# Kernel optimization log

Measured on AMD Instinct MI355X. Metric: run time of the kernel, lower is better.

Reference implementation:

```python
import jax, jax.numpy as jnp
import numpy as np

DIM = 384; HEADS = 12; WS = 7; SHIFT = 3
IMG_H = 56; IMG_W = 56; B = 32; MLP_HID = 1536
N = WS * WS; HEAD_DIM = DIM // HEADS


def _rel_pos_index():
    # standard Swin relative position index, shape [N, N], values in [0, (2*WS-1)^2)
    coords = np.stack(np.meshgrid(np.arange(WS), np.arange(WS), indexing='ij')).reshape(2, -1)
    rel = (coords[:, :, None] - coords[:, None, :]).transpose(1, 2, 0)
    rel[..., 0] += WS - 1
    rel[..., 1] += WS - 1
    rel[..., 0] *= 2 * WS - 1
    return jnp.asarray(rel.sum(-1))

REL_IDX = _rel_pos_index()


def _shift_mask():
    # Swin shifted-window attention mask: 0 within region, -100 across regions
    img = np.zeros((IMG_H, IMG_W))
    cnt = 0
    for hs in (slice(0, -WS), slice(-WS, -SHIFT), slice(-SHIFT, None)):
        for ws_ in (slice(0, -WS), slice(-WS, -SHIFT), slice(-SHIFT, None)):
            img[hs, ws_] = cnt
            cnt += 1
    mw = img.reshape(IMG_H // WS, WS, IMG_W // WS, WS).transpose(0, 2, 1, 3).reshape(-1, N)
    am = mw[:, None, :] - mw[:, :, None]
    return jnp.asarray(np.where(am != 0, -100.0, 0.0).astype(np.float32))


def setup_inputs() -> dict:
    key = jax.random.key(0)
    ks = jax.random.split(key, 8)
    rn = lambda k, s: jax.random.normal(k, s, jnp.float32) * 0.02
    return {
        'x': jax.random.normal(ks[0], (B, IMG_H * IMG_W, DIM), jnp.float32),
        'mask': _shift_mask(),
        'w_ln1': jnp.ones((DIM,), jnp.float32), 'b_ln1': jnp.zeros((DIM,), jnp.float32),
        'w_qkv': rn(ks[1], (3 * DIM, DIM)), 'b_qkv': jnp.zeros((3 * DIM,), jnp.float32),
        'rel_bias': rn(ks[2], ((2 * WS - 1) ** 2, HEADS)),
        'w_proj': rn(ks[3], (DIM, DIM)), 'b_proj': jnp.zeros((DIM,), jnp.float32),
        'w_ln2': jnp.ones((DIM,), jnp.float32), 'b_ln2': jnp.zeros((DIM,), jnp.float32),
        'w_fc1': rn(ks[4], (MLP_HID, DIM)), 'b_fc1': jnp.zeros((MLP_HID,), jnp.float32),
        'w_fc2': rn(ks[5], (DIM, MLP_HID)), 'b_fc2': jnp.zeros((DIM,), jnp.float32),
        'H': IMG_H, 'W': IMG_W,
    }


def _ln(x, g, b, eps=1e-5):
    mu = x.mean(-1, keepdims=True)
    var = ((x - mu) ** 2).mean(-1, keepdims=True)
    return (x - mu) * jax.lax.rsqrt(var + eps) * g + b


def reference(x, mask, w_ln1, b_ln1, w_qkv, b_qkv, rel_bias, w_proj, b_proj,
              w_ln2, b_ln2, w_fc1, b_fc1, w_fc2, b_fc2, H, W):
    Bsz, L, C = x.shape
    nW = (H // WS) * (W // WS)
    shortcut = x
    h = _ln(x, w_ln1, b_ln1).reshape(Bsz, H, W, C)
    # cyclic shift
    h = jnp.roll(h, (-SHIFT, -SHIFT), axis=(1, 2))
    # window partition -> [B*nW, N, C]
    h = h.reshape(Bsz, H // WS, WS, W // WS, WS, C).transpose(0, 1, 3, 2, 4, 5).reshape(-1, N, C)
    nB = h.shape[0]
    qkv = (h @ w_qkv.T + b_qkv).reshape(nB, N, 3, HEADS, HEAD_DIM).transpose(2, 0, 3, 1, 4)
    q, k, v = qkv[0] * (HEAD_DIM ** -0.5), qkv[1], qkv[2]  # each [nB, heads, N, hd]
    attn = jnp.einsum('bhnd,bhmd->bhnm', q, k)
    bias = rel_bias[REL_IDX].transpose(2, 0, 1)  # [heads, N, N]
    attn = attn + bias[None]
    attn = attn.reshape(Bsz, nW, HEADS, N, N) + mask[None, :, None]
    attn = jax.nn.softmax(attn, axis=-1).reshape(nB, HEADS, N, N)
    o = jnp.einsum('bhnm,bhmd->bhnd', attn, v).transpose(0, 2, 1, 3).reshape(nB, N, C)
    o = o @ w_proj.T + b_proj
    # window reverse
    o = o.reshape(Bsz, H // WS, W // WS, WS, WS, C).transpose(0, 1, 3, 2, 4, 5).reshape(Bsz, H, W, C)
    o = jnp.roll(o, (SHIFT, SHIFT), axis=(1, 2)).reshape(Bsz, H * W, C)
    x = shortcut + o
    h2 = _ln(x, w_ln2, b_ln2)
    h2 = jax.nn.gelu(h2 @ w_fc1.T + b_fc1) @ w_fc2.T + b_fc2
    return x + h2
```

## Files before the change

### kernel.cpp

```cpp
#include <hip/hip_runtime.h>
#include <stdint.h>

#define B_     32
#define IMG    56
#define L_     (IMG*IMG)
#define C_     384
#define HEADS_ 12
#define HD     32
#define WS_    7
#define N_     49
#define NWIN   64
#define NB     (B_*NWIN)
#define M_TOK  (NB*N_)
#define QKVF   1152

typedef __attribute__((ext_vector_type(8))) short bf16x8;
typedef __attribute__((ext_vector_type(4))) float f32x4;
typedef __attribute__((ext_vector_type(4))) unsigned short u16x4;

__device__ __forceinline__ float bf2f(unsigned short u) {
  union { unsigned int u; float f; } c; c.u = ((unsigned int)u) << 16; return c.f;
}
__device__ __forceinline__ unsigned short f2bf(float f) {
  union { float f; unsigned int u; } c; c.f = f;
  unsigned int r = c.u + 0x7FFFu + ((c.u >> 16) & 1u);
  return (unsigned short)(r >> 16);
}

__device__ __forceinline__ void gload_lds16(const void* g, void* l) {
  __builtin_amdgcn_global_load_lds(
      (const __attribute__((address_space(1))) unsigned int*)(uintptr_t)g,
      (__attribute__((address_space(3))) unsigned int*)(uintptr_t)l,
      16, 0, 0);
}

#define MFMA16(a, b, c) __builtin_amdgcn_mfma_f32_16x16x32_bf16((a), (b), (c), 0, 0, 0)

__global__ __launch_bounds__(256) void k_prep(
    const float* __restrict__ w_qkv, const float* __restrict__ w_proj,
    const float* __restrict__ w_fc1, const float* __restrict__ w_fc2,
    const float* __restrict__ relb,  const float* __restrict__ mask,
    ushort* __restrict__ wbq, ushort* __restrict__ wbp,
    ushort* __restrict__ wb1, ushort* __restrict__ wb2,
    ushort* __restrict__ bm)
{
  int g = blockIdx.x * 256 + threadIdx.x;
  if (g < 442368)        { wbq[g]            = f2bf(w_qkv[g]); return; }
  if (g < 589824)        { wbp[g - 442368]   = f2bf(w_proj[g - 442368]); return; }
  if (g < 1179648)       { wb1[g - 589824]   = f2bf(w_fc1[g - 589824]); return; }
  if (g < 1769472)       { wb2[g - 1179648]  = f2bf(w_fc2[g - 1179648]); return; }
  int n = g - 1769472;
  int r    = n & 3;
  int col  = (n >> 2) & 63;
  int quad = (n >> 8) & 3;
  int i    = (n >> 10) & 3;
  int hw   = n >> 12;
  int h = hw % HEADS_, wc = hw / HEADS_;
  int row = i * 16 + quad * 4 + r;
  float v;
  if (col >= N_) v = -30000.f;
  else if (row >= N_) v = 0.f;
  else {
    int idx = (row / WS_ - col / WS_ + 6) * 13 + (row % WS_ - col % WS_ + 6);
    v = relb[idx * HEADS_ + h] + mask[((size_t)wc * N_ + row) * N_ + col];
  }
  bm[n] = f2bf(v);
}

template<bool WINDOW>
__global__ __launch_bounds__(256) void k_ln(const float* __restrict__ X,
    const float* __restrict__ G, const float* __restrict__ Bb,
    ushort* __restrict__ out)
{
  int token = blockIdx.x * 4 + (threadIdx.x >> 6);
  int lane  = threadIdx.x & 63;
  const float* xp = X + (size_t)token * C_;
  float v[6];
#pragma unroll
  for (int t = 0; t < 6; t++) v[t] = xp[lane + 64*t];
  float s = 0.f, s2 = 0.f;
#pragma unroll
  for (int t = 0; t < 6; t++) { s += v[t]; s2 += v[t]*v[t]; }
#pragma unroll
  for (int off = 32; off > 0; off >>= 1) {
    s  += __shfl_down(s,  off, 64);
    s2 += __shfl_down(s2, off, 64);
  }
  s = __shfl(s, 0, 64); s2 = __shfl(s2, 0, 64);
  float mu   = s * (1.f / C_);
  float rstd = rsqrtf(s2 * (1.f / C_) - mu * mu + 1e-5f);
  size_t obase;
  if (WINDOW) {
    int b = token / L_, pix = token % L_;
    int hi = pix / IMG, wj = pix % IMG;
    int sh = hi - 3; if (sh < 0) sh += IMG;
    int sw = wj - 3; if (sw < 0) sw += IMG;
    int w = b * NWIN + (sh / WS_) * 8 + (sw / WS_);
    int p = (sh % WS_) * WS_ + (sw % WS_);
    obase = ((size_t)w * N_ + p) * C_;
  } else {
    obase = (size_t)token * C_;
  }
#pragma unroll
  for (int t = 0; t < 6; t++) {
    int c = lane + 64*t;
    out[obase + c] = f2bf((v[t] - mu) * rstd * G[c] + Bb[c]);
  }
}

template<int EPI, typename OutT>
__global__ __launch_bounds__(256, 2) void k_gemm(
    const ushort* __restrict__ A, const ushort* __restrict__ W,
    const float* __restrict__ bias, OutT* __restrict__ out,
    const float* __restrict__ res, int M, int N, int K)
{
  __shared__ __align__(16) ushort As[3][256*32];
  __shared__ __align__(16) ushort Bs[3][128*32];
  int ntn = N >> 7;
  int nwg = gridDim.x;
  int bid = (blockIdx.x & 7) * (nwg >> 3) + (blockIdx.x >> 3);
  int m0 = (bid / ntn) << 8;
  int n0 = (bid % ntn) << 7;
  int tid  = threadIdx.x;
  int wave = tid >> 6, lane = tid & 63;
  int l15  = lane & 15, quad = lane >> 4;
  int wm = (wave >> 1) << 7;
  int wn = (wave & 1) << 6;

  int srow = tid >> 2;
  int scol = (tid & 3) * 8;
  const ushort* gA = A + (size_t)(m0 + srow) * K + scol;
  const ushort* gB = W + (size_t)(n0 + srow) * K + scol;
  int oA = srow * 32 + scol;

  f32x4 acc[8][4];
#pragma unroll
  for (int i = 0; i < 8; i++)
#pragma unroll
    for (int j = 0; j < 4; j++) acc[i][j] = (f32x4){0.f, 0.f, 0.f, 0.f};

#pragma unroll
  for (int it = 0; it < 4; it++)
    gload_lds16(gA + (size_t)it * 64 * K, &As[0][oA + it * 2048]);
#pragma unroll
  for (int it = 0; it < 2; it++)
    gload_lds16(gB + (size_t)it * 64 * K, &Bs[0][oA + it * 2048]);
  gA += 32; gB += 32;
#pragma unroll
  for (int it = 0; it < 4; it++)
    gload_lds16(gA + (size_t)it * 64 * K, &As[1][oA + it * 2048]);
#pragma unroll
  for (int it = 0; it < 2; it++)
    gload_lds16(gB + (size_t)it * 64 * K, &Bs[1][oA + it * 2048]);
  gA += 32; gB += 32;

  int nt = K >> 5;
  int cur = 0, stg = 2;
  for (int t = 0; t < nt; t++) {
    if (t + 1 < nt) asm volatile("s_waitcnt vmcnt(6)" ::: "memory");
    else            asm volatile("s_waitcnt vmcnt(0)" ::: "memory");
    asm volatile("s_barrier" ::: "memory");
    if (t + 2 < nt) {
#pragma unroll
      for (int it = 0; it < 4; it++)
        gload_lds16(gA + (size_t)it * 64 * K, &As[stg][oA + it * 2048]);
#pragma unroll
      for (int it = 0; it < 2; it++)
        gload_lds16(gB + (size_t)it * 64 * K, &Bs[stg][oA + it * 2048]);
      gA += 32; gB += 32;
    }
    bf16x8 af[8], bfr[4];
#pragma unroll
    for (int i = 0; i < 8; i++) af[i]  = *(const bf16x8*)&As[cur][(wm + i*16 + l15)*32 + quad*8];
#pragma unroll
    for (int j = 0; j < 4; j++) bfr[j] = *(const bf16x8*)&Bs[cur][(wn + j*16 + l15)*32 + quad*8];
    __builtin_amdgcn_s_setprio(1);
#pragma unroll
    for (int i = 0; i < 8; i++)
#pragma unroll
      for (int j = 0; j < 4; j++)
        acc[i][j] = MFMA16(af[i], bfr[j], acc[i][j]);
    __builtin_amdgcn_s_setprio(0);
    cur = (cur == 2) ? 0 : cur + 1;
    stg = (stg == 2) ? 0 : stg + 1;
  }

  float bv[4];
#pragma unroll
  for (int j = 0; j < 4; j++) bv[j] = bias[n0 + wn + j*16 + l15];
#pragma unroll
  for (int i = 0; i < 8; i++) {
#pragma unroll
    for (int r = 0; r < 4; r++) {
      int row = m0 + wm + i*16 + quad*4 + r;
      size_t dstbase;
      if (EPI == 1) {
        int w = row / N_, p = row % N_;
        int b = w >> 6, wi = w & 63;
        int hi = (wi >> 3) * WS_ + p / WS_ + 3; if (hi >= IMG) hi -= IMG;
        int wj = (wi & 7)  * WS_ + p % WS_ + 3; if (wj >= IMG) wj -= IMG;
        dstbase = ((size_t)b * L_ + hi * IMG + wj) * C_;
      } else {
        dstbase = (size_t)row * N;
      }
#pragma unroll
      for (int j = 0; j < 4; j++) {
        int col = n0 + wn + j*16 + l15;
        float v = acc[i][j][r] + bv[j];
        if (EPI == 2) {
          float e = __expf(-1.5957691216057308f * (v + 0.044715f * v * v * v));
          v = v * __builtin_amdgcn_rcpf(1.f + e);
        }
        size_t dst = dstbase + col;
        if (EPI == 1) v += res[dst];
        if (EPI == 3) v += res[(size_t)row * N + col];
        if constexpr (sizeof(OutT) == 4) out[dst] = v;
        else                             out[dst] = f2bf(v);
      }
    }
  }
}

__global__ __launch_bounds__(256, 3) void k_attn_mfma(
    const ushort* __restrict__ qkv, const ushort* __restrict__ bm,
    ushort* __restrict__ out)
{
  __shared__ __align__(16) ushort Ps[4][64*64];
  __shared__ __align__(16) ushort Vt[4][32*64];
  int wave = threadIdx.x >> 6, lane = threadIdx.x & 63;
  int task = blockIdx.x * 4 + wave;
  int w = task / HEADS_, h = task % HEADS_;
  int l15 = lane & 15, quad = lane >> 4;

  const ushort* base = qkv + (size_t)w * N_ * QKVF + h * HD;

  bf16x8 qf[4], kf[4];
#pragma unroll
  for (int i = 0; i < 4; i++) {
    int rr = i * 16 + l15; if (rr > 48) rr = 48;
    const ushort* rp = base + (size_t)rr * QKVF + quad * 8;
    qf[i] = *(const bf16x8*)rp;
    kf[i] = *(const bf16x8*)(rp + C_);
  }

  {
    int m = lane > 48 ? 48 : lane;
    const ushort* vp = base + (size_t)m * QKVF + 2 * C_;
    bf16x8 v0 = *(const bf16x8*)vp;
    bf16x8 v1 = *(const bf16x8*)(vp + 8);
    bf16x8 v2 = *(const bf16x8*)(vp + 16);
    bf16x8 v3 = *(const bf16x8*)(vp + 24);
    ushort* vt = &Vt[wave][0];
#pragma unroll
    for (int d = 0; d < 32; d++) {
      ushort val = (ushort)(d < 8 ? v0[d & 7] : d < 16 ? v1[d & 7]
                                  : d < 24 ? v2[d & 7] : v3[d & 7]);
      vt[d * 64 + (lane ^ ((d & 7) << 3))] = val;
    }
  }

  f32x4 acc[4][4];
#pragma unroll
  for (int i = 0; i < 4; i++)
#pragma unroll
    for (int j = 0; j < 4; j++) acc[i][j] = (f32x4){0.f, 0.f, 0.f, 0.f};
#pragma unroll
  for (int i = 0; i < 4; i++)
#pragma unroll
    for (int j = 0; j < 4; j++)
      acc[i][j] = MFMA16(qf[i], kf[j], acc[i][j]);

  const ushort* bmb = bm + ((size_t)(w & 63) * HEADS_ + h) * 4096;
  float sv[4][4][4];
#pragma unroll
  for (int i = 0; i < 4; i++)
#pragma unroll
    for (int j = 0; j < 4; j++) {
      u16x4 bv = *(const u16x4*)(bmb + (((i * 4 + quad) * 64) + (j * 16 + l15)) * 4);
#pragma unroll
      for (int r = 0; r < 4; r++)
        sv[i][j][r] = acc[i][j][r] * 0.17677669529663687f + bf2f(bv[r]);
    }

  float mx[4][4], sm[4][4];
#pragma unroll
  for (int i = 0; i < 4; i++)
#pragma unroll
    for (int r = 0; r < 4; r++)
      mx[i][r] = fmaxf(fmaxf(sv[i][0][r], sv[i][1][r]),
                       fmaxf(sv[i][2][r], sv[i][3][r]));
#pragma unroll
  for (int off = 1; off <= 8; off <<= 1)
#pragma unroll
    for (int i = 0; i < 4; i++)
#pragma unroll
      for (int r = 0; r < 4; r++)
        mx[i][r] = fmaxf(mx[i][r], __shfl_xor(mx[i][r], off, 64));
#pragma unroll
  for (int i = 0; i < 4; i++)
#pragma unroll
    for (int r = 0; r < 4; r++) sm[i][r] = 0.f;
#pragma unroll
  for (int i = 0; i < 4; i++)
#pragma unroll
    for (int j = 0; j < 4; j++)
#pragma unroll
      for (int r = 0; r < 4; r++) {
        float e = __expf(sv[i][j][r] - mx[i][r]);
        sv[i][j][r] = e;
        sm[i][r] += e;
      }
#pragma unroll
  for (int off = 1; off <= 8; off <<= 1)
#pragma unroll
    for (int i = 0; i < 4; i++)
#pragma unroll
      for (int r = 0; r < 4; r++)
        sm[i][r] += __shfl_xor(sm[i][r], off, 64);

  ushort* pw = &Ps[wave][0];
#pragma unroll
  for (int i = 0; i < 4; i++)
#pragma unroll
    for (int r = 0; r < 4; r++) {
      float inv = __builtin_amdgcn_rcpf(sm[i][r]);
      int row = i * 16 + quad * 4 + r;
      int s = (row & 7) << 3;
#pragma unroll
      for (int j = 0; j < 4; j++)
        pw[row * 64 + ((j * 16 + l15) ^ s)] = f2bf(sv[i][j][r] * inv);
    }

  f32x4 o[4][2];
#pragma unroll
  for (int i = 0; i < 4; i++)
#pragma unroll
    for (int jv = 0; jv < 2; jv++) o[i][jv] = (f32x4){0.f, 0.f, 0.f, 0.f};
  const ushort* vt = &Vt[wave][0];
#pragma unroll
  for (int ks = 0; ks < 2; ks++) {
    int kc = ks * 32 + quad * 8;
    bf16x8 pa[4], vb[2];
#pragma unroll
    for (int i = 0; i < 4; i++) {
      int row = i * 16 + l15;
      pa[i] = *(const bf16x8*)&pw[row * 64 + (kc ^ ((row & 7) << 3))];
    }
#pragma unroll
    for (int jv = 0; jv < 2; jv++) {
      int nn = jv * 16 + l15;
      vb[jv] = *(const bf16x8*)&vt[nn * 64 + (kc ^ ((nn & 7) << 3))];
    }
#pragma unroll
    for (int i = 0; i < 4; i++)
#pragma unroll
      for (int jv = 0; jv < 2; jv++)
        o[i][jv] = MFMA16(pa[i], vb[jv], o[i][jv]);
  }

  ushort* op = out + ((size_t)w * N_) * C_ + h * HD;
#pragma unroll
  for (int i = 0; i < 4; i++)
#pragma unroll
    for (int r = 0; r < 4; r++) {
      int row = i * 16 + quad * 4 + r;
      if (row < N_) {
#pragma unroll
        for (int jv = 0; jv < 2; jv++)
          op[(size_t)row * C_ + jv * 16 + l15] = f2bf(o[i][jv][r]);
      }
    }
}

extern "C" void kernel_launch(void* const* d_in, const int* in_sizes, int n_in,
                              void* d_out, int out_size, void* d_ws, size_t ws_size,
                              hipStream_t stream) {
  (void)in_sizes; (void)n_in; (void)out_size; (void)ws_size;
  const float* x      = (const float*)d_in[0];
  const float* mask   = (const float*)d_in[1];
  const float* w_ln1  = (const float*)d_in[2];
  const float* b_ln1  = (const float*)d_in[3];
  const float* w_qkv  = (const float*)d_in[4];
  const float* b_qkv  = (const float*)d_in[5];
  const float* relb   = (const float*)d_in[6];
  const float* w_proj = (const float*)d_in[7];
  const float* b_proj = (const float*)d_in[8];
  const float* w_ln2  = (const float*)d_in[9];
  const float* b_ln2  = (const float*)d_in[10];
  const float* w_fc1  = (const float*)d_in[11];
  const float* b_fc1  = (const float*)d_in[12];
  const float* w_fc2  = (const float*)d_in[13];
  const float* b_fc2  = (const float*)d_in[14];

  char* ws = (char*)d_ws;
  ushort* r0 = (ushort*)ws;
  ushort* r1 = (ushort*)(ws + 308281344);
  ushort* bmt = (ushort*)(ws + 231211008);
  ushort* wbq = (ushort*)(ws + 385351680);
  ushort* wbp = wbq + QKVF * C_;
  ushort* wb1 = wbp + C_ * C_;
  ushort* wb2 = wb1 + 1536 * C_;
  float*  x1   = (float*)d_out;
  float*  outp = (float*)d_out;

  k_prep<<<4915200/256, 256, 0, stream>>>(w_qkv, w_proj, w_fc1, w_fc2,
                                          relb, mask, wbq, wbp, wb1, wb2, bmt);

  k_ln<true ><<<M_TOK/4, 256, 0, stream>>>(x, w_ln1, b_ln1, r1);
  k_gemm<0, ushort><<<(M_TOK/256)*(QKVF/128), 256, 0, stream>>>(
      r1, wbq, b_qkv, r0, nullptr, M_TOK, QKVF, 384);
  k_attn_mfma<<<NB*HEADS_/4, 256, 0, stream>>>(r0, bmt, r1);
  k_gemm<1, float><<<(M_TOK/256)*(C_/128), 256, 0, stream>>>(
      r1, wbp, b_proj, x1, x, M_TOK, C_, 384);
  k_ln<false><<<M_TOK/4, 256, 0, stream>>>(x1, w_ln2, b_ln2, r1);
  k_gemm<2, ushort><<<(M_TOK/256)*(1536/128), 256, 0, stream>>>(
      r1, wb1, b_fc1, r0, nullptr, M_TOK, 1536, 384);
  k_gemm<3, float><<<(M_TOK/256)*(C_/128), 256, 0, stream>>>(
      r0, wb2, b_fc2, outp, x1, M_TOK, C_, 1536);
}
```

Measured before the change: 1.030 ms.

## Load GEMM A operand directly from global into registers, bypassing LDS

The GEMM kernel no longer stages the A tile through shared memory. Each wave loads its A fragments straight from global memory into double-buffered registers, while B stays on a 3-stage LDS ring. This cuts LDS capacity and LDS read traffic for A and may raise occupancy. In exchange it adds register pressure and uncoalesced 16-byte global loads per lane, with hand-tuned vmcnt waits that must match the number of loads in flight.

```diff
diff --git a/kernel.cpp b/kernel.cpp
--- a/kernel.cpp
+++ b/kernel.cpp
@@ -114,7 +114,6 @@
     const float* __restrict__ bias, OutT* __restrict__ out,
     const float* __restrict__ res, int M, int N, int K)
 {
-  __shared__ __align__(16) ushort As[3][256*32];
   __shared__ __align__(16) ushort Bs[3][128*32];
   int ntn = N >> 7;
   int nwg = gridDim.x;
@@ -129,9 +128,10 @@
 
   int srow = tid >> 2;
   int scol = (tid & 3) * 8;
-  const ushort* gA = A + (size_t)(m0 + srow) * K + scol;
   const ushort* gB = W + (size_t)(n0 + srow) * K + scol;
-  int oA = srow * 32 + scol;
+  int oB = srow * 32 + scol;
+
+  const ushort* gA = A + (size_t)(m0 + wm + l15) * K + quad * 8;
 
   f32x4 acc[8][4];
 #pragma unroll
@@ -139,50 +139,93 @@
 #pragma unroll
     for (int j = 0; j < 4; j++) acc[i][j] = (f32x4){0.f, 0.f, 0.f, 0.f};
 
-#pragma unroll
-  for (int it = 0; it < 4; it++)
-    gload_lds16(gA + (size_t)it * 64 * K, &As[0][oA + it * 2048]);
-#pragma unroll
-  for (int it = 0; it < 2; it++)
-    gload_lds16(gB + (size_t)it * 64 * K, &Bs[0][oA + it * 2048]);
-  gA += 32; gB += 32;
-#pragma unroll
-  for (int it = 0; it < 4; it++)
-    gload_lds16(gA + (size_t)it * 64 * K, &As[1][oA + it * 2048]);
-#pragma unroll
-  for (int it = 0; it < 2; it++)
-    gload_lds16(gB + (size_t)it * 64 * K, &Bs[1][oA + it * 2048]);
-  gA += 32; gB += 32;
+  gload_lds16(gB,                     &Bs[0][oB]);
+  gload_lds16(gB + (size_t)64 * K,    &Bs[0][oB + 2048]);
+  gload_lds16(gB + 32,                &Bs[1][oB]);
+  gload_lds16(gB + (size_t)64 * K + 32, &Bs[1][oB + 2048]);
+  bf16x8 a0[8], a1[8];
+#pragma unroll
+  for (int i = 0; i < 8; i++) {
+    a0[i] = *(const bf16x8*)(gA + (size_t)(i * 16) * K);
+    a1[i] = *(const bf16x8*)(gA + (size_t)(i * 16) * K + 32);
+  }
+  asm volatile("s_waitcnt vmcnt(0)" ::: "memory");
+  asm volatile("s_barrier" ::: "memory");
 
   int nt = K >> 5;
-  int cur = 0, stg = 2;
-  for (int t = 0; t < nt; t++) {
-    if (t + 1 < nt) asm volatile("s_waitcnt vmcnt(6)" ::: "memory");
-    else            asm volatile("s_waitcnt vmcnt(0)" ::: "memory");
-    asm volatile("s_barrier" ::: "memory");
-    if (t + 2 < nt) {
-#pragma unroll
-      for (int it = 0; it < 4; it++)
-        gload_lds16(gA + (size_t)it * 64 * K, &As[stg][oA + it * 2048]);
-#pragma unroll
-      for (int it = 0; it < 2; it++)
-        gload_lds16(gB + (size_t)it * 64 * K, &Bs[stg][oA + it * 2048]);
-      gA += 32; gB += 32;
-    }
-    bf16x8 af[8], bfr[4];
-#pragma unroll
-    for (int i = 0; i < 8; i++) af[i]  = *(const bf16x8*)&As[cur][(wm + i*16 + l15)*32 + quad*8];
-#pragma unroll
-    for (int j = 0; j < 4; j++) bfr[j] = *(const bf16x8*)&Bs[cur][(wn + j*16 + l15)*32 + quad*8];
-    __builtin_amdgcn_s_setprio(1);
-#pragma unroll
-    for (int i = 0; i < 8; i++)
+  const ushort* gAn = gA + 64;
+  const ushort* gBn = gB + 64;
+  int rd = 0, wr = 2;
+
+  for (int t = 0; t < nt; t += 2) {
+    {
+      const ushort* bsrc = &Bs[0][0] + rd * 4096;
+      bf16x8 bfr[4];
 #pragma unroll
       for (int j = 0; j < 4; j++)
-        acc[i][j] = MFMA16(af[i], bfr[j], acc[i][j]);
-    __builtin_amdgcn_s_setprio(0);
-    cur = (cur == 2) ? 0 : cur + 1;
-    stg = (stg == 2) ? 0 : stg + 1;
+        bfr[j] = *(const bf16x8*)&bsrc[(wn + j*16 + l15)*32 + quad*8];
+      bool pre = (t + 2 < nt);
+      if (pre) {
+        ushort* bdst = &Bs[0][0] + wr * 4096 + oB;
+        gload_lds16(gBn,                  bdst);
+        gload_lds16(gBn + (size_t)64 * K, bdst + 2048);
+        gBn += 32;
+      }
+      asm volatile("" ::: "memory");
+      __builtin_amdgcn_s_setprio(1);
+#pragma unroll
+      for (int i = 0; i < 8; i++)
+#pragma unroll
+        for (int j = 0; j < 4; j++)
+          acc[i][j] = MFMA16(a0[i], bfr[j], acc[i][j]);
+      __builtin_amdgcn_s_setprio(0);
+      if (pre) {
+#pragma unroll
+        for (int i = 0; i < 8; i++)
+          a0[i] = *(const bf16x8*)(gAn + (size_t)(i * 16) * K);
+        gAn += 32;
+        asm volatile("s_waitcnt vmcnt(10)" ::: "memory");
+      } else {
+        asm volatile("s_waitcnt vmcnt(0)" ::: "memory");
+      }
+      asm volatile("s_barrier" ::: "memory");
+      rd = (rd == 2) ? 0 : rd + 1;
+      wr = (wr == 2) ? 0 : wr + 1;
+    }
+    {
+      const ushort* bsrc = &Bs[0][0] + rd * 4096;
+      bf16x8 bfr[4];
+#pragma unroll
+      for (int j = 0; j < 4; j++)
+        bfr[j] = *(const bf16x8*)&bsrc[(wn + j*16 + l15)*32 + quad*8];
+      bool pre = (t + 3 < nt);
+      if (pre) {
+        ushort* bdst = &Bs[0][0] + wr * 4096 + oB;
+        gload_lds16(gBn,                  bdst);
+        gload_lds16(gBn + (size_t)64 * K, bdst + 2048);
+        gBn += 32;
+      }
+      asm volatile("" ::: "memory");
+      __builtin_amdgcn_s_setprio(1);
+#pragma unroll
+      for (int i = 0; i < 8; i++)
+#pragma unroll
+        for (int j = 0; j < 4; j++)
+          acc[i][j] = MFMA16(a1[i], bfr[j], acc[i][j]);
+      __builtin_amdgcn_s_setprio(0);
+      if (pre) {
+#pragma unroll
+        for (int i = 0; i < 8; i++)
+          a1[i] = *(const bf16x8*)(gAn + (size_t)(i * 16) * K);
+        gAn += 32;
+        asm volatile("s_waitcnt vmcnt(10)" ::: "memory");
+      } else {
+        asm volatile("s_waitcnt vmcnt(0)" ::: "memory");
+      }
+      asm volatile("s_barrier" ::: "memory");
+      rd = (rd == 2) ? 0 : rd + 1;
+      wr = (wr == 2) ? 0 : wr + 1;
+    }
   }
 
   float bv[4];
```

After: 1.341 ms. +30.2%, slower.
